# Optimization experiments

Measured on AMD Instinct MI355X. Metric: run time of the kernel, lower is better.

Reference implementation:

```python
import jax, jax.numpy as jnp
import numpy as np
import math

B, N = 1, 512
C_S, C_Z, C_H, H = 384, 128, 16, 12
P_Q, P_V, NBINS = 4, 8, 64
OUT_DIM = H * (C_H + P_V * 4 + C_Z)


def setup_inputs() -> dict:
    key = jax.random.key(0)
    ks = jax.random.split(key, 16)
    def rn(k, shape, scale=1.0):
        return jax.random.normal(k, shape, dtype=jnp.float32) * scale
    rotations, _ = jnp.linalg.qr(rn(ks[3], (B, N, 3, 3)))  # orthogonal frames
    w = 0.02
    return {
        "s": rn(ks[0], (B, N, C_S)),
        "z": rn(ks[1], (B, N, N, C_Z)),
        "translations": rn(ks[2], (B, N, 3), 10.0),  # spread over ~0-32 A bins
        "rotations": rotations,
        "Wq": rn(ks[4], (C_S, H * C_H), w), "bq": jnp.zeros((H * C_H,), jnp.float32),
        "Wk": rn(ks[5], (C_S, H * C_H), w), "bk": jnp.zeros((H * C_H,), jnp.float32),
        "Wv": rn(ks[6], (C_S, H * C_H), w), "bv": jnp.zeros((H * C_H,), jnp.float32),
        "Wqp": rn(ks[7], (C_S, H * P_Q * 3), w), "bqp": jnp.zeros((H * P_Q * 3,), jnp.float32),
        "Wkp": rn(ks[8], (C_S, H * P_Q * 3), w), "bkp": jnp.zeros((H * P_Q * 3,), jnp.float32),
        "Wvp": rn(ks[9], (C_S, H * P_V * 3), w), "bvp": jnp.zeros((H * P_V * 3,), jnp.float32),
        "Wb": rn(ks[10], (C_Z, H), w), "bb": jnp.zeros((H,), jnp.float32),
        "emb": rn(ks[11], (NBINS, H), w),
        "scale_logits": jnp.zeros((3, H), jnp.float32),
        "head_weights": jnp.ones((H,), jnp.float32),
        "Wout": rn(ks[12], (OUT_DIM, C_S), w), "bout": jnp.zeros((C_S,), jnp.float32),
    }


def reference(s, z, translations, rotations, Wq, bq, Wk, bk, Wv, bv, Wqp, bqp, Wkp, bkp, Wvp, bvp, Wb, bb, emb, scale_logits, head_weights, Wout, bout):
    b, n, _ = s.shape
    t = translations
    q = (s @ Wq + bq).reshape(b, n, H, C_H)
    k = (s @ Wk + bk).reshape(b, n, H, C_H)
    v = (s @ Wv + bv).reshape(b, n, H, C_H)
    q_pts = (s @ Wqp + bqp).reshape(b, n, H, P_Q, 3)
    k_pts = (s @ Wkp + bkp).reshape(b, n, H, P_Q, 3)
    v_pts = (s @ Wvp + bvp).reshape(b, n, H, P_V, 3)
    # local -> global frame
    q_g = jnp.einsum('bnij,bnhpj->bnhpi', rotations, q_pts) + t[:, :, None, None, :]
    k_g = jnp.einsum('bnij,bnhpj->bnhpi', rotations, k_pts) + t[:, :, None, None, :]
    v_g = jnp.einsum('bnij,bnhpj->bnhpi', rotations, v_pts) + t[:, :, None, None, :]
    scalar_logits = jnp.einsum('bnhc,bmhc->bnmh', q, k) / math.sqrt(C_H)  # [b,n,m,h]
    point_dist = jnp.sum((q_g[:, :, None] - k_g[:, None]) ** 2, axis=-1)  # [b,n,m,h,p]
    point_logits = -0.5 * jnp.sum(point_dist, axis=-1) * head_weights[None, None, None, :]
    pair_bias = z @ Wb + bb  # [b,n,m,h]
    pair_dist = jnp.linalg.norm(t[:, :, None, :] - t[:, None, :, :], axis=-1)  # [b,n,m]
    edges = jnp.linspace(0.0, 32.0, NBINS + 1)
    bins = jnp.clip(jnp.searchsorted(edges, pair_dist, side='left') - 1, 0, NBINS - 1)
    dist_bias = emb[bins]  # [b,n,m,h]
    scales = jnp.stack([
        (pair_dist <= 5.0).astype(s.dtype),
        ((pair_dist > 5.0) & (pair_dist <= 15.0)).astype(s.dtype),
        jnp.ones_like(pair_dist),
    ], axis=-1)  # [b,n,m,3]
    per_head = jax.nn.softmax(scale_logits, axis=0)  # [3,h]
    multiscale = jnp.einsum('bnms,sh->bnmh', scales, per_head)
    logits = scalar_logits + point_logits + pair_bias + dist_bias + multiscale
    attn = jax.nn.softmax(logits.astype(jnp.float32), axis=2).astype(s.dtype)  # over m
    out_scalar = jnp.einsum('bnmh,bmhc->bnhc', attn, v)
    out_pts_g = jnp.einsum('bnmh,bmhpi->bnhpi', attn, v_g)
    # global -> local frame (R^T applied)
    out_pts_l = jnp.einsum('bnji,bnhpj->bnhpi', rotations, out_pts_g - t[:, :, None, None, :])
    out_norms = jnp.linalg.norm(out_pts_l, axis=-1)  # [b,n,h,p]
    pair_feat = jnp.einsum('bnmh,bnmc->bnhc', attn, z)
    feats = jnp.concatenate([
        out_scalar,
        out_pts_l.reshape(b, n, H, P_V * 3),
        out_norms,
        pair_feat,
    ], axis=-1).reshape(b, n, -1)  # [b,n,OUT_DIM]
    return feats @ Wout + bout
```

## Files before the change

### kernel.cpp

```cpp
#include <hip/hip_runtime.h>

#define NTOK 512
#define CS 384
#define CZ 128
#define CH 16
#define HN 12
#define PQ 4
#define PV 8
#define FEAT_DIM 2112
#define HSEG 176

__global__ __launch_bounds__(256) void k_proj(
    const float* __restrict__ s,
    const float* __restrict__ Wq,  const float* __restrict__ bq,
    const float* __restrict__ Wk,  const float* __restrict__ bk,
    const float* __restrict__ Wv,  const float* __restrict__ bv,
    const float* __restrict__ Wqp, const float* __restrict__ bqp,
    const float* __restrict__ Wkp, const float* __restrict__ bkp,
    const float* __restrict__ Wvp, const float* __restrict__ bvp,
    float* __restrict__ qs, float* __restrict__ ksT, float* __restrict__ vs,
    float* __restrict__ raw_g)
{
    __shared__ float s_l[16 * CS];
    __shared__ float Ws[16][64];
    const int t  = threadIdx.x;
    const int n0 = blockIdx.x * 16;

    const float4* sg  = (const float4*)(s + (size_t)n0 * CS);
    float4*       sl4 = (float4*)s_l;
#pragma unroll
    for (int j = 0; j < 6; ++j) sl4[j * 256 + t] = sg[j * 256 + t];

    const int col = blockIdx.y * 64 + (t & 63);
    const int tq  = t >> 6;
    const float* bv_;
    int lc;
    if (col < 192)      { bv_ = bq;  lc = col;       }
    else if (col < 384) { bv_ = bk;  lc = col - 192; }
    else if (col < 576) { bv_ = bv;  lc = col - 384; }
    else if (col < 720) { bv_ = bqp; lc = col - 576; }
    else if (col < 864) { bv_ = bkp; lc = col - 720; }
    else                { bv_ = bvp; lc = col - 864; }

    const int kk_s = t >> 4, cq = t & 15;
    const int gcol = blockIdx.y * 64 + cq * 4;
    const float* Wsrc; int lcs, ncs;
    if (gcol < 192)      { Wsrc = Wq;  lcs = gcol;       ncs = 192; }
    else if (gcol < 384) { Wsrc = Wk;  lcs = gcol - 192; ncs = 192; }
    else if (gcol < 576) { Wsrc = Wv;  lcs = gcol - 384; ncs = 192; }
    else if (gcol < 720) { Wsrc = Wqp; lcs = gcol - 576; ncs = 144; }
    else if (gcol < 864) { Wsrc = Wkp; lcs = gcol - 720; ncs = 144; }
    else                 { Wsrc = Wvp; lcs = gcol - 864; ncs = 288; }

    float a0, a1, a2, a3;
    a0 = a1 = a2 = a3 = bv_[lc];
    __syncthreads();

    for (int ks = 0; ks < CS; ks += 16) {
        float4 w4 = *(const float4*)&Wsrc[(size_t)(ks + kk_s) * ncs + lcs];
        __syncthreads();
        *(float4*)&Ws[kk_s][cq * 4] = w4;
        __syncthreads();
        const float* srow = s_l + tq * 4 * CS + ks;
#pragma unroll
        for (int kk = 0; kk < 16; ++kk) {
            float w = Ws[kk][t & 63];
            a0 += srow[kk] * w;
            a1 += srow[CS + kk] * w;
            a2 += srow[2 * CS + kk] * w;
            a3 += srow[3 * CS + kk] * w;
        }
    }

    const int n = n0 + tq * 4;
    if (col < 192) {
        qs[(size_t)(n + 0) * 192 + lc] = a0;
        qs[(size_t)(n + 1) * 192 + lc] = a1;
        qs[(size_t)(n + 2) * 192 + lc] = a2;
        qs[(size_t)(n + 3) * 192 + lc] = a3;
    } else if (col < 384) {
        float* p = ksT + (size_t)lc * NTOK + n;
        p[0] = a0; p[1] = a1; p[2] = a2; p[3] = a3;
    } else if (col < 576) {
        vs[(size_t)(n + 0) * 192 + lc] = a0;
        vs[(size_t)(n + 1) * 192 + lc] = a1;
        vs[(size_t)(n + 2) * 192 + lc] = a2;
        vs[(size_t)(n + 3) * 192 + lc] = a3;
    } else {
        const int pc = col - 576;
        raw_g[(size_t)(n + 0) * 576 + pc] = a0;
        raw_g[(size_t)(n + 1) * 576 + pc] = a1;
        raw_g[(size_t)(n + 2) * 576 + pc] = a2;
        raw_g[(size_t)(n + 3) * 576 + pc] = a3;
    }
}

__global__ __launch_bounds__(256) void k_frame(
    const float* __restrict__ raw_g,
    const float* __restrict__ trans,
    const float* __restrict__ rot,
    float* __restrict__ qg, float* __restrict__ kgT, float* __restrict__ vg,
    float* __restrict__ transT)
{
    const int e = blockIdx.x * 256 + threadIdx.x;
    if (e < 512 * 576) {
        const int n = e / 576, loc = e % 576;
        const int i = loc % 3, base = loc - i;
        const float* rp = raw_g + (size_t)n * 576 + base;
        float x0 = rp[0], x1 = rp[1], x2 = rp[2];
        const float* R = rot + (size_t)n * 9 + i * 3;
        float v = trans[(size_t)n * 3 + i] + R[0] * x0 + R[1] * x1 + R[2] * x2;
        if (loc < 144)      qg[(size_t)n * 144 + loc] = v;
        else if (loc < 288) kgT[(size_t)(loc - 144) * NTOK + n] = v;
        else                vg[(size_t)n * 288 + loc - 288] = v;
    } else {
        const int idx = e - 512 * 576;
        if (idx < 3 * NTOK) {
            const int m = idx / 3, i = idx % 3;
            transT[(size_t)i * NTOK + m] = trans[(size_t)m * 3 + i];
        }
    }
}

__global__ __launch_bounds__(256) void k_mid(
    const float* __restrict__ z,
    const float* __restrict__ qs, const float* __restrict__ ksT,
    const float* __restrict__ qg, const float* __restrict__ kgT,
    const float* __restrict__ trans, const float* __restrict__ transT,
    const float* __restrict__ Wb, const float* __restrict__ bbv,
    const float* __restrict__ emb, const float* __restrict__ slog,
    const float* __restrict__ hw,
    float* __restrict__ attn, float* __restrict__ feats)
{
    __shared__ float lg[HN * NTOK];
    __shared__ float zl[128 * 66];
    __shared__ float wbl[CZ * HN];
    __shared__ float embl[64 * HN];
    __shared__ float ql[192];
    __shared__ float qgl[144];
    __shared__ float tl[3];
    __shared__ float phl[36];
    __shared__ float hwl[HN];

    const int n = blockIdx.x, t = threadIdx.x;

    for (int i = t; i < CZ * HN; i += 256) wbl[i] = Wb[i];
    for (int i = t; i < 64 * HN; i += 256) embl[i] = emb[i];
    if (t < 192) ql[t] = qs[(size_t)n * 192 + t];
    if (t < 144) qgl[t] = qg[(size_t)n * 144 + t];
    if (t < 3)   tl[t] = trans[(size_t)n * 3 + t];
    if (t < HN)  hwl[t] = hw[t];
    if (t >= 64 && t < 64 + HN) {
        const int h = t - 64;
        float s0 = slog[h], s1 = slog[HN + h], s2 = slog[2 * HN + h];
        float mx = fmaxf(s0, fmaxf(s1, s2));
        float e0 = expf(s0 - mx), e1 = expf(s1 - mx), e2 = expf(s2 - mx);
        float inv = 1.f / (e0 + e1 + e2);
        phl[h] = e0 * inv; phl[12 + h] = e1 * inv; phl[24 + h] = e2 * inv;
    }

    const int ml = t & 63, hg = t >> 6, h0 = hg * 3;
    const float bb0 = bbv[h0], bb1 = bbv[h0 + 1], bb2 = bbv[h0 + 2];

    float4 pf[8];
    {
        const float4* zg = (const float4*)(z + (size_t)n * NTOK * CZ);
#pragma unroll
        for (int j = 0; j < 8; ++j) pf[j] = zg[j * 256 + t];
    }
    __syncthreads();

    for (int mc = 0; mc < 8; ++mc) {
#pragma unroll
        for (int j = 0; j < 8; ++j) {
            const int f = j * 256 + t;
            const int mm = f >> 5, c4 = (f & 31) * 4;
            float4 v = pf[j];
            zl[(c4 + 0) * 66 + mm] = v.x;
            zl[(c4 + 1) * 66 + mm] = v.y;
            zl[(c4 + 2) * 66 + mm] = v.z;
            zl[(c4 + 3) * 66 + mm] = v.w;
        }
        if (mc < 7) {
            const float4* zg = (const float4*)(z + ((size_t)n * NTOK + (mc + 1) * 64) * CZ);
#pragma unroll
            for (int j = 0; j < 8; ++j) pf[j] = zg[j * 256 + t];
        }
        __syncthreads();

        const int mg = mc * 64 + ml;
        float b0 = bb0, b1 = bb1, b2 = bb2;
        const float* zc = zl + ml;
#pragma unroll 8
        for (int c = 0; c < CZ; ++c) {
            float zv = zc[c * 66];
            const float* w = wbl + c * HN + h0;
            b0 += zv * w[0];
            b1 += zv * w[1];
            b2 += zv * w[2];
        }
        float dx = tl[0] - transT[mg];
        float dy = tl[1] - transT[NTOK + mg];
        float dz = tl[2] - transT[2 * NTOK + mg];
        float dist = sqrtf(dx * dx + dy * dy + dz * dz);
        int bin = min(63, max(0, (int)ceilf(dist * 2.f) - 1));
        const float in5  = (dist <= 5.f) ? 1.f : 0.f;
        const float in15 = (dist > 5.f && dist <= 15.f) ? 1.f : 0.f;

        float acc[3] = {b0, b1, b2};
#pragma unroll
        for (int k = 0; k < 3; ++k) {
            const int h = h0 + k;
            float sc = 0.f;
            const float* kk = ksT + (size_t)h * CH * NTOK + mg;
            const float* qq = ql + h * CH;
#pragma unroll
            for (int c = 0; c < CH; ++c) sc += qq[c] * kk[(size_t)c * NTOK];
            float sd = 0.f;
            const float* kg = kgT + (size_t)h * 12 * NTOK + mg;
            const float* qp = qgl + h * 12;
#pragma unroll
            for (int i = 0; i < 12; ++i) {
                float d = qp[i] - kg[(size_t)i * NTOK];
                sd += d * d;
            }
            acc[k] += sc * 0.25f - 0.5f * sd * hwl[h]
                    + embl[bin * HN + h]
                    + phl[24 + h] + in5 * phl[h] + in15 * phl[12 + h];
        }
        lg[(h0 + 0) * NTOK + mg] = acc[0];
        lg[(h0 + 1) * NTOK + mg] = acc[1];
        lg[(h0 + 2) * NTOK + mg] = acc[2];
        __syncthreads();
    }

    const int lane = t & 63;
#pragma unroll
    for (int hh = 0; hh < 3; ++hh) {
        const int h = hg * 3 + hh;
        float* row = lg + h * NTOK;
        float v[8];
        float mx = -1e30f;
#pragma unroll
        for (int i = 0; i < 8; ++i) { v[i] = row[lane + 64 * i]; mx = fmaxf(mx, v[i]); }
#pragma unroll
        for (int off = 32; off; off >>= 1) mx = fmaxf(mx, __shfl_xor(mx, off));
        float sm = 0.f;
#pragma unroll
        for (int i = 0; i < 8; ++i) { v[i] = expf(v[i] - mx); sm += v[i]; }
#pragma unroll
        for (int off = 32; off; off >>= 1) sm += __shfl_xor(sm, off);
        const float inv = 1.f / sm;
        float* arow = attn + ((size_t)n * HN + h) * NTOK;
#pragma unroll
        for (int i = 0; i < 8; ++i) {
            float a = v[i] * inv;
            row[lane + 64 * i] = a;
            arow[lane + 64 * i] = a;
        }
    }
    __syncthreads();

    const int slab = t >> 6;
    const int c2 = (t & 63) * 2;
    float pacc[HN][2];
#pragma unroll
    for (int h = 0; h < HN; ++h) { pacc[h][0] = 0.f; pacc[h][1] = 0.f; }
    const float* zp = z + (size_t)n * NTOK * CZ + (size_t)slab * 128 * CZ + c2;
    const float* ap = lg + slab * 128;
#pragma unroll 4
    for (int m = 0; m < 128; ++m) {
        float2 zv = *(const float2*)(zp + (size_t)m * CZ);
#pragma unroll
        for (int h = 0; h < HN; ++h) {
            float a = ap[h * NTOK + m];
            pacc[h][0] += a * zv.x;
            pacc[h][1] += a * zv.y;
        }
    }
    float* out_l = zl;
    for (int s = 0; s < 4; ++s) {
        __syncthreads();
        if (slab == s) {
#pragma unroll
            for (int h = 0; h < HN; ++h) {
                float* p = &out_l[h * CZ + c2];
                if (s == 0) { p[0] = pacc[h][0]; p[1] = pacc[h][1]; }
                else        { p[0] += pacc[h][0]; p[1] += pacc[h][1]; }
            }
        }
    }
    __syncthreads();
    for (int i = t; i < HN * CZ; i += 256) {
        const int h = i >> 7, c = i & 127;
        feats[(size_t)n * FEAT_DIM + h * HSEG + 48 + c] = out_l[i];
    }
}

__global__ __launch_bounds__(256) void k_outmm(
    const float* __restrict__ attn,
    const float* __restrict__ vs, const float* __restrict__ vg,
    const float* __restrict__ trans,
    const float* __restrict__ rot,
    float* __restrict__ feats)
{
    __shared__ float As_t[64][33];
    __shared__ float Vs[64][40];
    __shared__ float out_l[32 * 40];
    __shared__ float Rl[32][9];
    __shared__ float tl[32][3];
    const int t   = threadIdx.x;
    const int gn0 = blockIdx.x * 32;
    const int h   = blockIdx.y;

    const int slab  = t >> 6;
    const int w     = t & 63;
    const int n0l   = (w >> 3) * 4;
    const int j0    = (w & 7) * 5;

    float acc[4][5];
#pragma unroll
    for (int i = 0; i < 4; ++i)
#pragma unroll
        for (int k = 0; k < 5; ++k) acc[i][k] = 0.f;

    for (int step = 0; step < 8; ++step) {
        const int mb = step * 64;
        __syncthreads();
#pragma unroll
        for (int jj = 0; jj < 2; ++jj) {
            const int f = t + jj * 256;
            const int n_loc = f >> 4, c4 = f & 15;
            float4 a = *(const float4*)&attn[(((size_t)(gn0 + n_loc)) * HN + h) * NTOK + mb + c4 * 4];
            As_t[c4 * 4 + 0][n_loc] = a.x;
            As_t[c4 * 4 + 1][n_loc] = a.y;
            As_t[c4 * 4 + 2][n_loc] = a.z;
            As_t[c4 * 4 + 3][n_loc] = a.w;
        }
#pragma unroll
        for (int jj = 0; jj < 10; ++jj) {
            const int f = t + jj * 256;
            const int m_loc = f / 40, jv = f % 40;
            float v;
            if (jv < 16) v = vs[(size_t)(mb + m_loc) * 192 + h * 16 + jv];
            else         v = vg[(size_t)(mb + m_loc) * 288 + h * 24 + (jv - 16)];
            Vs[m_loc][jv] = v;
        }
        __syncthreads();
#pragma unroll
        for (int mi = 0; mi < 16; ++mi) {
            const int m = slab * 16 + mi;
            float4 a = *(const float4*)&As_t[m][n0l];
            float vv[5];
#pragma unroll
            for (int k = 0; k < 5; ++k) vv[k] = Vs[m][j0 + k];
            const float av[4] = {a.x, a.y, a.z, a.w};
#pragma unroll
            for (int i = 0; i < 4; ++i)
#pragma unroll
                for (int k = 0; k < 5; ++k)
                    acc[i][k] += av[i] * vv[k];
        }
    }

    for (int s = 0; s < 4; ++s) {
        __syncthreads();
        if (slab == s) {
#pragma unroll
            for (int i = 0; i < 4; ++i)
#pragma unroll
                for (int k = 0; k < 5; ++k) {
                    float* p = &out_l[(n0l + i) * 40 + j0 + k];
                    if (s == 0) *p = acc[i][k];
                    else        *p += acc[i][k];
                }
        }
    }
    for (int i = t; i < 32 * 12; i += 256) {
        const int n_loc = i / 12, r = i % 12;
        if (r < 9) Rl[n_loc][r] = rot[(size_t)(gn0 + n_loc) * 9 + r];
        else       tl[n_loc][r - 9] = trans[(size_t)(gn0 + n_loc) * 3 + (r - 9)];
    }
    __syncthreads();

    for (int f = t; f < 32 * 48; f += 256) {
        const int n_loc = f / 48, j = f % 48;
        const float* sh = &out_l[n_loc * 40];
        float* fp = feats + (size_t)(gn0 + n_loc) * FEAT_DIM + h * HSEG;
        const float* R = Rl[n_loc];
        const float* tv = tl[n_loc];
        if (j < 16) {
            fp[j] = sh[j];
        } else if (j < 40) {
            const int jj = j - 16, p = jj / 3, i = jj % 3;
            float val = 0.f;
#pragma unroll
            for (int q = 0; q < 3; ++q) val += R[q * 3 + i] * (sh[16 + p * 3 + q] - tv[q]);
            fp[16 + jj] = val;
        } else {
            const int p = j - 40;
            float s2 = 0.f;
#pragma unroll
            for (int i = 0; i < 3; ++i) {
                float val = 0.f;
#pragma unroll
                for (int q = 0; q < 3; ++q) val += R[q * 3 + i] * (sh[16 + p * 3 + q] - tv[q]);
                s2 += val * val;
            }
            fp[40 + p] = sqrtf(s2);
        }
    }
}

#define KT 16
__global__ __launch_bounds__(256) void k_outproj(
    const float* __restrict__ feats,
    const float* __restrict__ Wout,
    const float* __restrict__ bout,
    float* __restrict__ out)
{
    __shared__ float As[KT][64];
    __shared__ float Bs[KT][64];
    const int t  = threadIdx.x;
    const int n0 = blockIdx.x * 64;
    const int j0 = blockIdx.y * 64;
    const int k0 = blockIdx.z * HSEG;

    const int arow = t >> 2, akq = (t & 3) * 4;
    const int bkk  = t >> 4, bjq = (t & 15) * 4;
    const int tr   = t >> 4, tc  = t & 15;

    float acc[4][4] = {{0.f}};
    for (int s = 0; s < 11; ++s) {
        const int ks = k0 + s * KT;
        float4 a4 = *(const float4*)&feats[(size_t)(n0 + arow) * FEAT_DIM + ks + akq];
        float4 b4 = *(const float4*)&Wout[(size_t)(ks + bkk) * 384 + j0 + bjq];
        __syncthreads();
        As[akq + 0][arow] = a4.x;
        As[akq + 1][arow] = a4.y;
        As[akq + 2][arow] = a4.z;
        As[akq + 3][arow] = a4.w;
        *(float4*)&Bs[bkk][bjq] = b4;
        __syncthreads();
#pragma unroll
        for (int kk = 0; kk < KT; ++kk) {
            float4 av = *(const float4*)&As[kk][tr * 4];
            float4 bv = *(const float4*)&Bs[kk][tc * 4];
            acc[0][0] += av.x * bv.x; acc[0][1] += av.x * bv.y;
            acc[0][2] += av.x * bv.z; acc[0][3] += av.x * bv.w;
            acc[1][0] += av.y * bv.x; acc[1][1] += av.y * bv.y;
            acc[1][2] += av.y * bv.z; acc[1][3] += av.y * bv.w;
            acc[2][0] += av.z * bv.x; acc[2][1] += av.z * bv.y;
            acc[2][2] += av.z * bv.z; acc[2][3] += av.z * bv.w;
            acc[3][0] += av.w * bv.x; acc[3][1] += av.w * bv.y;
            acc[3][2] += av.w * bv.z; acc[3][3] += av.w * bv.w;
        }
    }

    const bool addb = (blockIdx.z == 0);
#pragma unroll
    for (int i = 0; i < 4; ++i) {
        const int row = n0 + tr * 4 + i;
#pragma unroll
        for (int jj = 0; jj < 4; ++jj) {
            const int col = j0 + tc * 4 + jj;
            float v = acc[i][jj];
            if (addb) v += bout[col];
            atomicAdd(&out[(size_t)row * 384 + col], v);
        }
    }
}

extern "C" void kernel_launch(void* const* d_in, const int* in_sizes, int n_in,
                              void* d_out, int out_size, void* d_ws, size_t ws_size,
                              hipStream_t stream) {
    const float* s     = (const float*)d_in[0];
    const float* z     = (const float*)d_in[1];
    const float* trans = (const float*)d_in[2];
    const float* rot   = (const float*)d_in[3];
    const float* Wq    = (const float*)d_in[4];
    const float* bq    = (const float*)d_in[5];
    const float* Wk    = (const float*)d_in[6];
    const float* bk    = (const float*)d_in[7];
    const float* Wv    = (const float*)d_in[8];
    const float* bv    = (const float*)d_in[9];
    const float* Wqp   = (const float*)d_in[10];
    const float* bqp   = (const float*)d_in[11];
    const float* Wkp   = (const float*)d_in[12];
    const float* bkp   = (const float*)d_in[13];
    const float* Wvp   = (const float*)d_in[14];
    const float* bvp   = (const float*)d_in[15];
    const float* Wb    = (const float*)d_in[16];
    const float* bb    = (const float*)d_in[17];
    const float* emb   = (const float*)d_in[18];
    const float* slog  = (const float*)d_in[19];
    const float* hw    = (const float*)d_in[20];
    const float* Wout  = (const float*)d_in[21];
    const float* bout  = (const float*)d_in[22];

    float* W = (float*)d_ws;
    float* qs     = W;
    float* ksT    = qs + 98304;
    float* vs     = ksT + 98304;
    float* qg     = vs + 98304;
    float* kgT    = qg + 73728;
    float* vg     = kgT + 73728;
    float* transT = vg + 147456;
    float* attn   = transT + 1536;
    float* feats  = attn + 3145728;
    float* raw_g  = feats + 1081344;

    k_proj<<<dim3(32, 18), 256, 0, stream>>>(s, Wq, bq, Wk, bk, Wv, bv,
                                             Wqp, bqp, Wkp, bkp, Wvp, bvp,
                                             qs, ksT, vs, raw_g);
    k_frame<<<1158, 256, 0, stream>>>(raw_g, trans, rot, qg, kgT, vg, transT);
    k_mid<<<512, 256, 0, stream>>>(z, qs, ksT, qg, kgT, trans, transT,
                                   Wb, bb, emb, slog, hw, attn, feats);
    k_outmm<<<dim3(16, 12), 256, 0, stream>>>(attn, vs, vg, trans, rot, feats);
    hipMemsetAsync(d_out, 0, (size_t)NTOK * 384 * sizeof(float), stream);
    k_outproj<<<dim3(8, 6, 12), 256, 0, stream>>>(feats, Wout, bout, (float*)d_out);
}
```

Measured before the change: 398.9 us.

## Transpose shared-memory layouts in k_mid for vectorized float4 LDS reads

Changes the shared-memory layouts inside k_mid. The z tile is stored row-major with padding rather than transposed, Wb is stored transposed per head, and the logits/attention buffer is stored m-major with the 12 heads contiguous. The pair-bias dot product and the attention-times-z accumulation can then use float4 LDS loads in place of scalar strided ones, cutting LDS instruction count. The trade-off is strided, possibly bank-conflicting LDS access in the softmax pass and a different bank pattern for the row-major z reads.

Measured after the change: 412.2 us. +3.3%, slower.

```diff
diff --git a/kernel.cpp b/kernel.cpp
--- a/kernel.cpp
+++ b/kernel.cpp
@@ -132,9 +132,9 @@
     const float* __restrict__ hw,
     float* __restrict__ attn, float* __restrict__ feats)
 {
-    __shared__ float lg[HN * NTOK];
-    __shared__ float zl[128 * 66];
-    __shared__ float wbl[CZ * HN];
+    __shared__ __align__(16) float lgT[NTOK * HN];
+    __shared__ __align__(16) float zl[64 * 132];
+    __shared__ __align__(16) float wbT[HN * CZ];
     __shared__ float embl[64 * HN];
     __shared__ float ql[192];
     __shared__ float qgl[144];
@@ -144,7 +144,10 @@
 
     const int n = blockIdx.x, t = threadIdx.x;
 
-    for (int i = t; i < CZ * HN; i += 256) wbl[i] = Wb[i];
+    for (int i = t; i < CZ * HN; i += 256) {
+        const int h = i >> 7, c = i & 127;
+        wbT[h * CZ + c] = Wb[(size_t)c * HN + h];
+    }
     for (int i = t; i < 64 * HN; i += 256) embl[i] = emb[i];
     if (t < 192) ql[t] = qs[(size_t)n * 192 + t];
     if (t < 144) qgl[t] = qg[(size_t)n * 144 + t];
@@ -170,16 +173,16 @@
     }
     __syncthreads();
 
+    const float* w0 = wbT + (h0 + 0) * CZ;
+    const float* w1 = wbT + (h0 + 1) * CZ;
+    const float* w2 = wbT + (h0 + 2) * CZ;
+
     for (int mc = 0; mc < 8; ++mc) {
 #pragma unroll
         for (int j = 0; j < 8; ++j) {
             const int f = j * 256 + t;
-            const int mm = f >> 5, c4 = (f & 31) * 4;
-            float4 v = pf[j];
-            zl[(c4 + 0) * 66 + mm] = v.x;
-            zl[(c4 + 1) * 66 + mm] = v.y;
-            zl[(c4 + 2) * 66 + mm] = v.z;
-            zl[(c4 + 3) * 66 + mm] = v.w;
+            const int row = f >> 5, c4 = (f & 31) * 4;
+            *(float4*)&zl[row * 132 + c4] = pf[j];
         }
         if (mc < 7) {
             const float4* zg = (const float4*)(z + ((size_t)n * NTOK + (mc + 1) * 64) * CZ);
@@ -190,14 +193,16 @@
 
         const int mg = mc * 64 + ml;
         float b0 = bb0, b1 = bb1, b2 = bb2;
-        const float* zc = zl + ml;
-#pragma unroll 8
-        for (int c = 0; c < CZ; ++c) {
-            float zv = zc[c * 66];
-            const float* w = wbl + c * HN + h0;
-            b0 += zv * w[0];
-            b1 += zv * w[1];
-            b2 += zv * w[2];
+        const float* zrow = zl + ml * 132;
+#pragma unroll 4
+        for (int cq = 0; cq < CZ; cq += 4) {
+            float4 zv = *(const float4*)&zrow[cq];
+            float4 v0 = *(const float4*)&w0[cq];
+            float4 v1 = *(const float4*)&w1[cq];
+            float4 v2 = *(const float4*)&w2[cq];
+            b0 += zv.x * v0.x + zv.y * v0.y + zv.z * v0.z + zv.w * v0.w;
+            b1 += zv.x * v1.x + zv.y * v1.y + zv.z * v1.z + zv.w * v1.w;
+            b2 += zv.x * v2.x + zv.y * v2.y + zv.z * v2.z + zv.w * v2.w;
         }
         float dx = tl[0] - transT[mg];
         float dy = tl[1] - transT[NTOK + mg];
@@ -228,21 +233,23 @@
                     + embl[bin * HN + h]
                     + phl[24 + h] + in5 * phl[h] + in15 * phl[12 + h];
         }
-        lg[(h0 + 0) * NTOK + mg] = acc[0];
-        lg[(h0 + 1) * NTOK + mg] = acc[1];
-        lg[(h0 + 2) * NTOK + mg] = acc[2];
+        lgT[mg * HN + h0 + 0] = acc[0];
+        lgT[mg * HN + h0 + 1] = acc[1];
+        lgT[mg * HN + h0 + 2] = acc[2];
         __syncthreads();
     }
 
     const int lane = t & 63;
 #pragma unroll
     for (int hh = 0; hh < 3; ++hh) {
-        const int h = hg * 3 + hh;
-        float* row = lg + h * NTOK;
+        const int h = h0 + hh;
         float v[8];
         float mx = -1e30f;
 #pragma unroll
-        for (int i = 0; i < 8; ++i) { v[i] = row[lane + 64 * i]; mx = fmaxf(mx, v[i]); }
+        for (int i = 0; i < 8; ++i) {
+            v[i] = lgT[(lane + 64 * i) * HN + h];
+            mx = fmaxf(mx, v[i]);
+        }
 #pragma unroll
         for (int off = 32; off; off >>= 1) mx = fmaxf(mx, __shfl_xor(mx, off));
         float sm = 0.f;
@@ -255,7 +262,7 @@
 #pragma unroll
         for (int i = 0; i < 8; ++i) {
             float a = v[i] * inv;
-            row[lane + 64 * i] = a;
+            lgT[(lane + 64 * i) * HN + h] = a;
             arow[lane + 64 * i] = a;
         }
     }
@@ -267,16 +274,25 @@
 #pragma unroll
     for (int h = 0; h < HN; ++h) { pacc[h][0] = 0.f; pacc[h][1] = 0.f; }
     const float* zp = z + (size_t)n * NTOK * CZ + (size_t)slab * 128 * CZ + c2;
-    const float* ap = lg + slab * 128;
+    const float* lp = lgT + slab * 128 * HN;
 #pragma unroll 4
     for (int m = 0; m < 128; ++m) {
         float2 zv = *(const float2*)(zp + (size_t)m * CZ);
-#pragma unroll
-        for (int h = 0; h < HN; ++h) {
-            float a = ap[h * NTOK + m];
-            pacc[h][0] += a * zv.x;
-            pacc[h][1] += a * zv.y;
-        }
+        float4 a0 = *(const float4*)&lp[m * HN + 0];
+        float4 a1 = *(const float4*)&lp[m * HN + 4];
+        float4 a2 = *(const float4*)&lp[m * HN + 8];
+        pacc[0][0]  += a0.x * zv.x;  pacc[0][1]  += a0.x * zv.y;
+        pacc[1][0]  += a0.y * zv.x;  pacc[1][1]  += a0.y * zv.y;
+        pacc[2][0]  += a0.z * zv.x;  pacc[2][1]  += a0.z * zv.y;
+        pacc[3][0]  += a0.w * zv.x;  pacc[3][1]  += a0.w * zv.y;
+        pacc[4][0]  += a1.x * zv.x;  pacc[4][1]  += a1.x * zv.y;
+        pacc[5][0]  += a1.y * zv.x;  pacc[5][1]  += a1.y * zv.y;
+        pacc[6][0]  += a1.z * zv.x;  pacc[6][1]  += a1.z * zv.y;
+        pacc[7][0]  += a1.w * zv.x;  pacc[7][1]  += a1.w * zv.y;
+        pacc[8][0]  += a2.x * zv.x;  pacc[8][1]  += a2.x * zv.y;
+        pacc[9][0]  += a2.y * zv.x;  pacc[9][1]  += a2.y * zv.y;
+        pacc[10][0] += a2.z * zv.x;  pacc[10][1] += a2.z * zv.y;
+        pacc[11][0] += a2.w * zv.x;  pacc[11][1] += a2.w * zv.y;
     }
     float* out_l = zl;
     for (int s = 0; s < 4; ++s) {
```
